# Kernel tuning notes

Hardware: AMD Instinct MI355X
Metric: run time of the kernel (lower is better)

Reference implementation:

```python
import math
import jax, jax.numpy as jnp
import numpy as np

B, S, HID = 2, 1024, 1024
NH, HD = 16, 64
WIN = 4096
CACHE = 3072
EPS = 1e-5


def _clinear(xr, xi, Wr, Wi, br, bi):
    # complex linear: (xr + i xi)(Wr + i Wi)^T + (br + i bi)
    yr = xr @ Wr.T - xi @ Wi.T + br
    yi = xr @ Wi.T + xi @ Wr.T + bi
    return yr, yi


def _forward(hidden_re, hidden_im, K_cache_re, K_cache_im, V_cache_re, V_cache_im,
             gamma, beta_re, beta_im,
             q_Wr, q_Wi, q_br, q_bi, k_Wr, k_Wi, k_br, k_bi,
             v_Wr, v_Wi, v_br, v_bi, o_Wr, o_Wi, o_br, o_bi):
    batch, seq, _ = hidden_re.shape
    # --- complex LayerNorm: center complex mean, normalize by sqrt(E|x-mu|^2) ---
    mur = hidden_re.mean(-1, keepdims=True)
    mui = hidden_im.mean(-1, keepdims=True)
    cr = hidden_re - mur
    ci = hidden_im - mui
    inv = jax.lax.rsqrt((cr * cr + ci * ci).mean(-1, keepdims=True) + EPS)
    nr = cr * inv * gamma + beta_re
    ni = ci * inv * gamma + beta_im
    # --- projections ---
    Qr, Qi = _clinear(nr, ni, q_Wr, q_Wi, q_br, q_bi)
    Kr, Ki = _clinear(nr, ni, k_Wr, k_Wi, k_br, k_bi)
    Vr, Vi = _clinear(nr, ni, v_Wr, v_Wi, v_br, v_bi)
    Qr = Qr.reshape(batch, seq, NH, HD)
    Qi = Qi.reshape(batch, seq, NH, HD)
    Kr = Kr.reshape(batch, seq, NH, HD)
    Ki = Ki.reshape(batch, seq, NH, HD)
    Vr = Vr.reshape(batch, seq, NH, HD)
    Vi = Vi.reshape(batch, seq, NH, HD)
    # --- KV cache concat + window eviction (static shapes) ---
    cache_len = K_cache_re.shape[1]
    Kr = jnp.concatenate([K_cache_re, Kr], axis=1)
    Ki = jnp.concatenate([K_cache_im, Ki], axis=1)
    Vr = jnp.concatenate([V_cache_re, Vr], axis=1)
    Vi = jnp.concatenate([V_cache_im, Vi], axis=1)
    total_kv = Kr.shape[1]
    if total_kv > WIN:
        drop = total_kv - WIN
        Kr, Ki, Vr, Vi = Kr[:, drop:], Ki[:, drop:], Vr[:, drop:], Vi[:, drop:]
        cache_len = max(0, cache_len - drop)
        total_kv = WIN
    # --- Hermitian scores: Re(Q K^H) = Qr.Kr + Qi.Ki ---
    scale = 1.0 / math.sqrt(HD)
    scores = (jnp.einsum('bshd,bthd->bhst', Qr, Kr)
              + jnp.einsum('bshd,bthd->bhst', Qi, Ki)) * scale
    rows = jnp.arange(seq)[:, None]
    cols = jnp.arange(total_kv)[None, :]
    allowed = cols <= rows + cache_len  # causal within current chunk, full cache visible
    scores = jnp.where(allowed, scores, jnp.float32(-1e30))
    weights = jax.nn.softmax(scores, axis=-1)  # [B,NH,S,T]
    outr = jnp.einsum('bhst,bthd->bshd', weights, Vr).reshape(batch, seq, NH * HD)
    outi = jnp.einsum('bhst,bthd->bshd', weights, Vi).reshape(batch, seq, NH * HD)
    dr, di = _clinear(outr, outi, o_Wr, o_Wi, o_br, o_bi)
    out_re = hidden_re + dr
    out_im = hidden_im + di
    new_K_re, new_K_im = Kr[:, -WIN:], Ki[:, -WIN:]
    new_V_re, new_V_im = Vr[:, -WIN:], Vi[:, -WIN:]
    return out_re, out_im, new_K_re, new_K_im, new_V_re, new_V_im


def setup_inputs() -> dict:
    key = jax.random.key(0)
    ks = jax.random.split(key, 16)
    w = 0.02
    d = {
        'hidden_re': jax.random.normal(ks[0], (B, S, HID), jnp.float32),
        'hidden_im': jax.random.normal(ks[1], (B, S, HID), jnp.float32),
        'K_cache_re': jax.random.normal(ks[2], (B, CACHE, NH, HD), jnp.float32),
        'K_cache_im': jax.random.normal(ks[3], (B, CACHE, NH, HD), jnp.float32),
        'V_cache_re': jax.random.normal(ks[4], (B, CACHE, NH, HD), jnp.float32),
        'V_cache_im': jax.random.normal(ks[5], (B, CACHE, NH, HD), jnp.float32),
        'gamma': jnp.ones((HID,), jnp.float32),
        'beta_re': jnp.zeros((HID,), jnp.float32),
        'beta_im': jnp.zeros((HID,), jnp.float32),
    }
    for i, p in enumerate(['q', 'k', 'v', 'o']):
        d[p + '_Wr'] = jax.random.normal(ks[6 + 2 * i], (HID, HID), jnp.float32) * w
        d[p + '_Wi'] = jax.random.normal(ks[7 + 2 * i], (HID, HID), jnp.float32) * w
        d[p + '_br'] = jnp.zeros((HID,), jnp.float32)
        d[p + '_bi'] = jnp.zeros((HID,), jnp.float32)
    return d


def reference(hidden_re, hidden_im, K_cache_re, K_cache_im, V_cache_re, V_cache_im,
              gamma, beta_re, beta_im,
              q_Wr, q_Wi, q_br, q_bi, k_Wr, k_Wi, k_br, k_bi,
              v_Wr, v_Wi, v_br, v_bi, o_Wr, o_Wi, o_br, o_bi):
    return _forward(hidden_re, hidden_im, K_cache_re, K_cache_im, V_cache_re, V_cache_im,
                    gamma, beta_re, beta_im,
                    q_Wr, q_Wi, q_br, q_bi, k_Wr, k_Wi, k_br, k_bi,
                    v_Wr, v_Wi, v_br, v_bi, o_Wr, o_Wi, o_br, o_bi)
```

## Files before the change

kernel.cpp:

```cpp
#include <hip/hip_runtime.h>
#include <hip/hip_bf16.h>
#include <cstdint>
#include <cstddef>

typedef __bf16 bf16x8 __attribute__((ext_vector_type(8)));
typedef float  f32x4  __attribute__((ext_vector_type(4)));

__device__ __forceinline__ unsigned short f2bf(float f) {
  union { float f; unsigned u; } v; v.f = f;
  unsigned u = v.u;
  u += 0x7FFFu + ((u >> 16) & 1u);
  return (unsigned short)(u >> 16);
}

struct alignas(16) US8 { unsigned short u[8]; };

__device__ __forceinline__ void g2lds16(const void* g, void* l) {
  __builtin_amdgcn_global_load_lds(
      (const __attribute__((address_space(1))) unsigned int*)g,
      (__attribute__((address_space(3))) unsigned int*)l, 16, 0, 0);
}

#define BB 2
#define SS 1024
#define HID 1024
#define NHH 16
#define HDD 64
#define TT 4096
#define CCH 3072

__global__ __launch_bounds__(256) void ln_kernel(
    const float* __restrict__ hre, const float* __restrict__ him,
    const float* __restrict__ gamma, const float* __restrict__ bre,
    const float* __restrict__ bim, unsigned short* __restrict__ Aln)
{
  int m = blockIdx.x;
  int tid = threadIdx.x;
  const float4 vr = ((const float4*)(hre + (size_t)m * HID))[tid];
  const float4 vi = ((const float4*)(him + (size_t)m * HID))[tid];
  float sr = vr.x + vr.y + vr.z + vr.w;
  float si = vi.x + vi.y + vi.z + vi.w;
  float sq = vr.x*vr.x + vr.y*vr.y + vr.z*vr.z + vr.w*vr.w
           + vi.x*vi.x + vi.y*vi.y + vi.z*vi.z + vi.w*vi.w;
  __shared__ float red[3][4];
  int lane = tid & 63, w = tid >> 6;
  for (int off = 32; off; off >>= 1) {
    sr += __shfl_down(sr, off, 64);
    si += __shfl_down(si, off, 64);
    sq += __shfl_down(sq, off, 64);
  }
  if (lane == 0) { red[0][w] = sr; red[1][w] = si; red[2][w] = sq; }
  __syncthreads();
  sr = red[0][0] + red[0][1] + red[0][2] + red[0][3];
  si = red[1][0] + red[1][1] + red[1][2] + red[1][3];
  sq = red[2][0] + red[2][1] + red[2][2] + red[2][3];
  float mur = sr * (1.f/1024.f), mui = si * (1.f/1024.f);
  float var = sq * (1.f/1024.f) - mur*mur - mui*mui;
  float inv = rsqrtf(var + 1e-5f);
  int k = tid * 4;
  float4 g  = ((const float4*)gamma)[tid];
  float4 br = ((const float4*)bre)[tid];
  float4 bi = ((const float4*)bim)[tid];
  ushort4 nr, ni;
  nr.x = f2bf((vr.x - mur) * inv * g.x + br.x);
  nr.y = f2bf((vr.y - mur) * inv * g.y + br.y);
  nr.z = f2bf((vr.z - mur) * inv * g.z + br.z);
  nr.w = f2bf((vr.w - mur) * inv * g.w + br.w);
  ni.x = f2bf((vi.x - mui) * inv * g.x + bi.x);
  ni.y = f2bf((vi.y - mui) * inv * g.y + bi.y);
  ni.z = f2bf((vi.z - mui) * inv * g.z + bi.z);
  ni.w = f2bf((vi.w - mui) * inv * g.w + bi.w);
  *(ushort4*)&Aln[(size_t)m * 2048 + k]        = nr;
  *(ushort4*)&Aln[(size_t)m * 2048 + 1024 + k] = ni;
}

__global__ __launch_bounds__(256) void wprep_kernel(
    const float* __restrict__ qWr, const float* __restrict__ qWi,
    const float* __restrict__ kWr, const float* __restrict__ kWi,
    const float* __restrict__ vWr, const float* __restrict__ vWi,
    const float* __restrict__ oWr, const float* __restrict__ oWi,
    unsigned short* __restrict__ Wc)
{
  int gid = blockIdx.x * 256 + threadIdx.x;
  int idx = gid * 8;
  int p   = idx >> 22;
  int rem = idx & 0x3FFFFF;
  int n   = rem >> 11;
  int k   = rem & 2047;
  const float* Wr; const float* Wi;
  switch (p) {
    case 0:  Wr = qWr; Wi = qWi; break;
    case 1:  Wr = kWr; Wi = kWi; break;
    case 2:  Wr = vWr; Wi = vWi; break;
    default: Wr = oWr; Wi = oWi; break;
  }
  const float* src; float sgn = 1.f;
  if (n < 1024) {
    if (k < 1024) src = Wr + (size_t)n * 1024 + k;
    else        { src = Wi + (size_t)n * 1024 + (k - 1024); sgn = -1.f; }
  } else {
    if (k < 1024) src = Wi + (size_t)(n - 1024) * 1024 + k;
    else          src = Wr + (size_t)(n - 1024) * 1024 + (k - 1024);
  }
  float4 a = ((const float4*)src)[0];
  float4 b = ((const float4*)src)[1];
  US8 o;
  o.u[0] = f2bf(a.x * sgn); o.u[1] = f2bf(a.y * sgn);
  o.u[2] = f2bf(a.z * sgn); o.u[3] = f2bf(a.w * sgn);
  o.u[4] = f2bf(b.x * sgn); o.u[5] = f2bf(b.y * sgn);
  o.u[6] = f2bf(b.z * sgn); o.u[7] = f2bf(b.w * sgn);
  *(US8*)&Wc[idx] = o;
}

__global__ __launch_bounds__(256) void bprep_kernel(
    const float* __restrict__ qbr, const float* __restrict__ qbi,
    const float* __restrict__ kbr, const float* __restrict__ kbi,
    const float* __restrict__ vbr, const float* __restrict__ vbi,
    const float* __restrict__ obr, const float* __restrict__ obi,
    float* __restrict__ bc)
{
  int idx = blockIdx.x * 256 + threadIdx.x;
  int p = idx >> 11, n = idx & 2047;
  const float* br; const float* bi;
  switch (p) {
    case 0:  br = qbr; bi = qbi; break;
    case 1:  br = kbr; bi = kbi; break;
    case 2:  br = vbr; bi = vbi; break;
    default: br = obr; bi = obi; break;
  }
  bc[idx] = (n < 1024) ? br[n] : bi[n - 1024];
}

__global__ __launch_bounds__(256) void gemm_bt_kernel(
    const unsigned short* __restrict__ A, const unsigned short* __restrict__ Bm,
    const float* __restrict__ bias, float* __restrict__ C, int Nstride, int K)
{
  __shared__ alignas(16) unsigned short As[128][32];
  __shared__ alignas(16) unsigned short Bs[128][32];
  int bm = blockIdx.y * 128;
  int bn = blockIdx.x * 128;
  int tid = threadIdx.x;
  int lane = tid & 63, w = tid >> 6;
  int wm = (w >> 1) * 64, wn = (w & 1) * 64;
  int l15 = lane & 15, q = lane >> 4;
  int lr = tid >> 2;
  int lc = (tid & 3) * 8;

  f32x4 acc[4][4] = {};

  for (int k0 = 0; k0 < K; k0 += 32) {
    *(float4*)&As[lr][lc]    = *(const float4*)&A [(size_t)(bm + lr)      * K + k0 + lc];
    *(float4*)&As[lr+64][lc] = *(const float4*)&A [(size_t)(bm + lr + 64) * K + k0 + lc];
    *(float4*)&Bs[lr][lc]    = *(const float4*)&Bm[(size_t)(bn + lr)      * K + k0 + lc];
    *(float4*)&Bs[lr+64][lc] = *(const float4*)&Bm[(size_t)(bn + lr + 64) * K + k0 + lc];
    __syncthreads();
    bf16x8 af[4], bfr[4];
#pragma unroll
    for (int i = 0; i < 4; i++) af[i]  = *(const bf16x8*)&As[wm + i*16 + l15][q*8];
#pragma unroll
    for (int i = 0; i < 4; i++) bfr[i] = *(const bf16x8*)&Bs[wn + i*16 + l15][q*8];
#pragma unroll
    for (int i = 0; i < 4; i++)
#pragma unroll
      for (int j = 0; j < 4; j++)
        acc[i][j] = __builtin_amdgcn_mfma_f32_16x16x32_bf16(af[i], bfr[j], acc[i][j], 0, 0, 0);
    __syncthreads();
  }

#pragma unroll
  for (int i = 0; i < 4; i++)
#pragma unroll
    for (int j = 0; j < 4; j++) {
      int n = bn + wn + j*16 + l15;
      float bv = bias[n];
#pragma unroll
      for (int r = 0; r < 4; r++) {
        int m = bm + wm + i*16 + q*4 + r;
        C[(size_t)m * Nstride + n] = acc[i][j][r] + bv;
      }
    }
}

__global__ __launch_bounds__(256) void gemm_oproj_kernel(
    const unsigned short* __restrict__ A, const unsigned short* __restrict__ Bm,
    const float* __restrict__ bias, const float* __restrict__ hre,
    const float* __restrict__ him, float* __restrict__ out)
{
  __shared__ alignas(16) unsigned short As[128][32];
  __shared__ alignas(16) unsigned short Bs[128][32];
  int bm = blockIdx.y * 128;
  int bn = blockIdx.x * 128;
  int tid = threadIdx.x;
  int lane = tid & 63, w = tid >> 6;
  int wm = (w >> 1) * 64, wn = (w & 1) * 64;
  int l15 = lane & 15, q = lane >> 4;
  int lr = tid >> 2;
  int lc = (tid & 3) * 8;
  const int K = 2048;

  f32x4 acc[4][4] = {};

  for (int k0 = 0; k0 < K; k0 += 32) {
    *(float4*)&As[lr][lc]    = *(const float4*)&A [(size_t)(bm + lr)      * K + k0 + lc];
    *(float4*)&As[lr+64][lc] = *(const float4*)&A [(size_t)(bm + lr + 64) * K + k0 + lc];
    *(float4*)&Bs[lr][lc]    = *(const float4*)&Bm[(size_t)(bn + lr)      * K + k0 + lc];
    *(float4*)&Bs[lr+64][lc] = *(const float4*)&Bm[(size_t)(bn + lr + 64) * K + k0 + lc];
    __syncthreads();
    bf16x8 af[4], bfr[4];
#pragma unroll
    for (int i = 0; i < 4; i++) af[i]  = *(const bf16x8*)&As[wm + i*16 + l15][q*8];
#pragma unroll
    for (int i = 0; i < 4; i++) bfr[i] = *(const bf16x8*)&Bs[wn + i*16 + l15][q*8];
#pragma unroll
    for (int i = 0; i < 4; i++)
#pragma unroll
      for (int j = 0; j < 4; j++)
        acc[i][j] = __builtin_amdgcn_mfma_f32_16x16x32_bf16(af[i], bfr[j], acc[i][j], 0, 0, 0);
    __syncthreads();
  }

#pragma unroll
  for (int i = 0; i < 4; i++)
#pragma unroll
    for (int j = 0; j < 4; j++) {
      int n = bn + wn + j*16 + l15;
      float bv = bias[n];
#pragma unroll
      for (int r = 0; r < 4; r++) {
        int m = bm + wm + i*16 + q*4 + r;
        float val = acc[i][j][r] + bv;
        if (n < 1024) out[(size_t)m * 1024 + n] = val + hre[(size_t)m * 1024 + n];
        else out[2097152 + (size_t)m * 1024 + (n - 1024)] = val + him[(size_t)m * 1024 + (n - 1024)];
      }
    }
}

__global__ __launch_bounds__(256) void pack_q_kernel(
    const float* __restrict__ Cqkv, unsigned short* __restrict__ Qp)
{
  int gid = blockIdx.x * 256 + threadIdx.x;
  int idx = gid * 4;
  int d2 = idx & 127;
  int s  = (idx >> 7) & 1023;
  int bh = idx >> 17;
  int b = bh >> 4, h = bh & 15;
  int d = d2 & 63;
  int col = (d2 < 64) ? (h*64 + d) : (1024 + h*64 + d);
  float4 v = *(const float4*)&Cqkv[((size_t)b * 1024 + s) * 6144 + col];
  ushort4 o;
  o.x = f2bf(v.x * 0.125f); o.y = f2bf(v.y * 0.125f);
  o.z = f2bf(v.z * 0.125f); o.w = f2bf(v.w * 0.125f);
  *(ushort4*)&Qp[idx] = o;
}

__global__ __launch_bounds__(256) void pack_kv_kernel(
    const float* __restrict__ c_re, const float* __restrict__ c_im,
    const float* __restrict__ Cqkv, int colbase,
    unsigned short* __restrict__ Kp,
    float* __restrict__ out_re, float* __restrict__ out_im)
{
  int gid = blockIdx.x * 256 + threadIdx.x;
  int idx = gid * 4;
  int d2 = idx & 127;
  int t  = (idx >> 7) & 4095;
  int bh = idx >> 19;
  int b = bh >> 4, h = bh & 15;
  int d = d2 & 63;
  bool im = d2 >= 64;
  float4 v;
  if (t < CCH) {
    const float* src = im ? c_im : c_re;
    v = *(const float4*)&src[(((size_t)b * CCH + t) * 16 + h) * 64 + d];
  } else {
    int col = colbase + (im ? (1024 + h*64 + d) : (h*64 + d));
    v = *(const float4*)&Cqkv[((size_t)b * 1024 + (t - CCH)) * 6144 + col];
  }
  if (Kp) {
    ushort4 o;
    o.x = f2bf(v.x); o.y = f2bf(v.y); o.z = f2bf(v.z); o.w = f2bf(v.w);
    *(ushort4*)&Kp[idx] = o;
  }
  float* dst = im ? out_im : out_re;
  *(float4*)&dst[(((size_t)b * 4096 + t) * 16 + h) * 64 + d] = v;
}

__global__ __launch_bounds__(256) void pack_vt_kernel(
    const float* __restrict__ Vc_re, const float* __restrict__ Vc_im,
    const float* __restrict__ Cqkv, unsigned short* __restrict__ Vt)
{
  __shared__ float Ts[64][136];
  const int ty = blockIdx.x & 63;
  const int bh = blockIdx.x >> 6;
  const int b = bh >> 4, h = bh & 15;
  const int t0 = ty * 64;
  const int tid = threadIdx.x;
#pragma unroll
  for (int rr = 0; rr < 8; rr++) {
    int j = rr * 256 + tid;
    int t_loc = j >> 5, c = j & 31;
    int d2 = c * 4;
    int t = t0 + t_loc;
    float4 v;
    if (t < CCH) {
      const float* src = (d2 < 64) ? Vc_re : Vc_im;
      int d = (d2 < 64) ? d2 : d2 - 64;
      v = *(const float4*)&src[(((size_t)b * CCH + t) * 16 + h) * 64 + d];
    } else {
      int col = 4096 + ((d2 < 64) ? (h*64 + d2) : (1024 + h*64 + d2 - 64));
      v = *(const float4*)&Cqkv[((size_t)b * 1024 + (t - CCH)) * 6144 + col];
    }
    *(float4*)&Ts[t_loc][d2] = v;
  }
  __syncthreads();
  const int d2 = tid >> 1, half = tid & 1;
  unsigned short tmp[32];
#pragma unroll
  for (int i = 0; i < 32; i++) tmp[i] = f2bf(Ts[half*32 + i][d2]);
  size_t dst = (size_t)bh * 128 * 4096 + (size_t)d2 * 4096 + t0 + half*32;
#pragma unroll
  for (int kq = 0; kq < 4; kq++)
    *(US8*)&Vt[dst + kq*8] = *(US8*)&tmp[kq*8];
}

__global__ __launch_bounds__(256) void attn_kernel(
    const unsigned short* __restrict__ Qp, const unsigned short* __restrict__ Kp,
    const unsigned short* __restrict__ Vt, float* __restrict__ Opart,
    float* __restrict__ Lpart)
{
  const int bh   = blockIdx.x;
  const int sblk = blockIdx.y;
  const int tpar = blockIdx.z;
  const int s0 = sblk * 128;
  const int tid = threadIdx.x;
  const int lane = tid & 63, w = tid >> 6;
  const int l15 = lane & 15, q = lane >> 4;

  __shared__ alignas(16) unsigned short Ks[2][64][128];
  __shared__ alignas(16) unsigned short Vs[2][128][64];
  __shared__ alignas(16) unsigned short Ps[4][32][64];

  bf16x8 qf[2][4];
#pragma unroll
  for (int mi = 0; mi < 2; mi++) {
    const size_t qb = ((size_t)bh * 1024 + s0 + w*32 + mi*16 + l15) * 128;
#pragma unroll
    for (int kc = 0; kc < 4; kc++)
      qf[mi][kc] = *(const bf16x8*)&Qp[qb + kc*32 + q*8];
  }

  f32x4 oacc[2][8] = {};
  float lsum[2][4] = {};

  const size_t kpb = (size_t)bh * 4096 * 128;
  const size_t vtb = (size_t)bh * 128 * 4096;
  const int n_tiles = 2*sblk + 50;
  const int n_safe  = n_tiles - 2;

  auto issue = [&](int buf, int t0) {
#pragma unroll
    for (int kk = 0; kk < 4; kk++) {
      int j = (w*4 + kk)*64 + lane;
      int r = j >> 4, p = j & 15, c = p ^ (r & 7);
      g2lds16(&Kp[kpb + (size_t)(t0 + r) * 128 + c*8],
              (unsigned short*)&Ks[buf][0][0] + (size_t)j * 8);
    }
#pragma unroll
    for (int kk = 0; kk < 4; kk++) {
      int j = (w*4 + kk)*64 + lane;
      int r = j >> 3, p = j & 7, c = p ^ (r & 7);
      g2lds16(&Vt[vtb + (size_t)r * 4096 + t0 + c*8],
              (unsigned short*)&Vs[buf][0][0] + (size_t)j * 8);
    }
  };

  int buf = 0;
  issue(0, tpar * 64);

  for (int it = tpar; it < n_tiles; it += 2) {
    __syncthreads();
    if (it + 2 < n_tiles) issue(buf ^ 1, (it + 2) * 64);

    f32x4 sacc[2][4] = {};
#pragma unroll
    for (int kc = 0; kc < 4; kc++) {
      bf16x8 kf[4];
#pragma unroll
      for (int nc = 0; nc < 4; nc++)
        kf[nc] = *(const bf16x8*)&Ks[buf][nc*16 + l15][((kc*4 + q) ^ (l15 & 7)) * 8];
#pragma unroll
      for (int mi = 0; mi < 2; mi++)
#pragma unroll
        for (int nc = 0; nc < 4; nc++)
          sacc[mi][nc] = __builtin_amdgcn_mfma_f32_16x16x32_bf16(qf[mi][kc], kf[nc], sacc[mi][nc], 0, 0, 0);
    }

    const bool safe = (it < n_safe);
    const int t0 = it << 6;
#pragma unroll
    for (int mi = 0; mi < 2; mi++)
#pragma unroll
      for (int r = 0; r < 4; r++) {
        const int rr = mi*16 + q*4 + r;
        const int rel = s0 + w*32 + rr + CCH - t0;
        float ls = 0.f;
#pragma unroll
        for (int nc = 0; nc < 4; nc++) {
          float p = __expf(sacc[mi][nc][r]);
          if (!safe && (nc*16 + l15 > rel)) p = 0.f;
          ls += p;
          int cch = ((nc*2 + (l15 >> 3)) ^ (rr & 7));
          Ps[w][rr][cch*8 + (l15 & 7)] = f2bf(p);
        }
        lsum[mi][r] += ls;
      }

#pragma unroll
    for (int kch = 0; kch < 2; kch++) {
      bf16x8 pf[2];
#pragma unroll
      for (int mi = 0; mi < 2; mi++) {
        int rr = mi*16 + l15;
        pf[mi] = *(const bf16x8*)&Ps[w][rr][((kch*4 + q) ^ (rr & 7)) * 8];
      }
#pragma unroll
      for (int dc = 0; dc < 8; dc++) {
        int d2 = dc*16 + l15;
        bf16x8 vfr = *(const bf16x8*)&Vs[buf][d2][((kch*4 + q) ^ (l15 & 7)) * 8];
#pragma unroll
        for (int mi = 0; mi < 2; mi++)
          oacc[mi][dc] = __builtin_amdgcn_mfma_f32_16x16x32_bf16(pf[mi], vfr, oacc[mi][dc], 0, 0, 0);
      }
    }
    buf ^= 1;
  }

  const size_t pb = ((size_t)tpar * 32 + bh) * 1024 + s0 + w*32;
#pragma unroll
  for (int mi = 0; mi < 2; mi++)
#pragma unroll
    for (int r = 0; r < 4; r++) {
      float l = lsum[mi][r];
      l += __shfl_xor(l, 1, 64);
      l += __shfl_xor(l, 2, 64);
      l += __shfl_xor(l, 4, 64);
      l += __shfl_xor(l, 8, 64);
      if (l15 == 0) Lpart[pb + mi*16 + q*4 + r] = l;
    }
#pragma unroll
  for (int mi = 0; mi < 2; mi++)
#pragma unroll
    for (int dc = 0; dc < 8; dc++)
#pragma unroll
      for (int r = 0; r < 4; r++)
        Opart[(pb + mi*16 + q*4 + r) * 128 + dc*16 + l15] = oacc[mi][dc][r];
}

__global__ __launch_bounds__(256) void attn_combine_kernel(
    const float* __restrict__ Opart, const float* __restrict__ Lpart,
    unsigned short* __restrict__ Ao)
{
  const size_t TS = 4194304ull;
  int gid = blockIdx.x * 256 + threadIdx.x;
  int idx = gid * 8;
  int m = idx >> 11, n0 = idx & 2047;
  int b = m >> 10, s = m & 1023;
  int h, d2_0;
  if (n0 < 1024) { h = n0 >> 6; d2_0 = n0 & 63; }
  else { h = (n0 - 1024) >> 6; d2_0 = 64 + ((n0 - 1024) & 63); }
  int bh = b*16 + h;
  size_t ob = ((size_t)bh * 1024 + s) * 128 + d2_0;
  float l0 = Lpart[(size_t)bh * 1024 + s];
  float l1 = Lpart[TS/128 + (size_t)bh * 1024 + s];
  float inv = 1.f / (l0 + l1);
  float4 x0 = *(const float4*)&Opart[ob];
  float4 x1 = *(const float4*)&Opart[ob + 4];
  float4 y0 = *(const float4*)&Opart[ob + TS];
  float4 y1 = *(const float4*)&Opart[ob + TS + 4];
  US8 o;
  o.u[0] = f2bf((x0.x + y0.x) * inv); o.u[1] = f2bf((x0.y + y0.y) * inv);
  o.u[2] = f2bf((x0.z + y0.z) * inv); o.u[3] = f2bf((x0.w + y0.w) * inv);
  o.u[4] = f2bf((x1.x + y1.x) * inv); o.u[5] = f2bf((x1.y + y1.y) * inv);
  o.u[6] = f2bf((x1.z + y1.z) * inv); o.u[7] = f2bf((x1.w + y1.w) * inv);
  *(US8*)&Ao[idx] = o;
}

extern "C" void kernel_launch(void* const* d_in, const int* in_sizes, int n_in,
                              void* d_out, int out_size, void* d_ws, size_t ws_size,
                              hipStream_t stream)
{
  (void)in_sizes; (void)n_in; (void)out_size; (void)ws_size;
  const float* hre = (const float*)d_in[0];
  const float* him = (const float*)d_in[1];
  const float* Kcr = (const float*)d_in[2];
  const float* Kci = (const float*)d_in[3];
  const float* Vcr = (const float*)d_in[4];
  const float* Vci = (const float*)d_in[5];
  const float* gamma = (const float*)d_in[6];
  const float* bre = (const float*)d_in[7];
  const float* bim = (const float*)d_in[8];
  const float* qWr = (const float*)d_in[9];
  const float* qWi = (const float*)d_in[10];
  const float* qbr = (const float*)d_in[11];
  const float* qbi = (const float*)d_in[12];
  const float* kWr = (const float*)d_in[13];
  const float* kWi = (const float*)d_in[14];
  const float* kbr = (const float*)d_in[15];
  const float* kbi = (const float*)d_in[16];
  const float* vWr = (const float*)d_in[17];
  const float* vWi = (const float*)d_in[18];
  const float* vbr = (const float*)d_in[19];
  const float* vbi = (const float*)d_in[20];
  const float* oWr = (const float*)d_in[21];
  const float* oWi = (const float*)d_in[22];
  const float* obr = (const float*)d_in[23];
  const float* obi = (const float*)d_in[24];
  float* out = (float*)d_out;

  char* ws = (char*)d_ws;
  size_t off = 0;
  auto carve = [&](size_t bytes) {
    char* p = ws + off;
    off += (bytes + 255) & ~(size_t)255;
    return p;
  };
  unsigned short* Aln = (unsigned short*)carve(2048ull * 2048 * 2);
  unsigned short* Wc  = (unsigned short*)carve(4ull * 2048 * 2048 * 2);
  float*          bc  = (float*)carve(4ull * 2048 * 4);
  float*          Cqkv= (float*)carve(2048ull * 6144 * 4);
  unsigned short* Qp  = (unsigned short*)carve(4194304ull * 2);
  unsigned short* Kp  = (unsigned short*)carve(16777216ull * 2);
  unsigned short* Vt  = (unsigned short*)carve(16777216ull * 2);
  unsigned short* Ao  = (unsigned short*)carve(2048ull * 2048 * 2);

  float* Opart = (float*)Cqkv;
  float* Lpart = (float*)Aln;

  float* out_Kre = out + 4194304;
  float* out_Kim = out + 4194304 + 8388608;
  float* out_Vre = out + 4194304 + 2 * 8388608;
  float* out_Vim = out + 4194304 + 3 * 8388608;

  hipLaunchKernelGGL(ln_kernel, dim3(2048), dim3(256), 0, stream,
                     hre, him, gamma, bre, bim, Aln);
  hipLaunchKernelGGL(wprep_kernel, dim3(8192), dim3(256), 0, stream,
                     qWr, qWi, kWr, kWi, vWr, vWi, oWr, oWi, Wc);
  hipLaunchKernelGGL(bprep_kernel, dim3(32), dim3(256), 0, stream,
                     qbr, qbi, kbr, kbi, vbr, vbi, obr, obi, bc);
  hipLaunchKernelGGL(gemm_bt_kernel, dim3(48, 16), dim3(256), 0, stream,
                     Aln, Wc, bc, Cqkv, 6144, 2048);
  hipLaunchKernelGGL(pack_q_kernel, dim3(4096), dim3(256), 0, stream, Cqkv, Qp);
  hipLaunchKernelGGL(pack_kv_kernel, dim3(16384), dim3(256), 0, stream,
                     Kcr, Kci, Cqkv, 2048, Kp, out_Kre, out_Kim);
  hipLaunchKernelGGL(pack_kv_kernel, dim3(16384), dim3(256), 0, stream,
                     Vcr, Vci, Cqkv, 4096, (unsigned short*)nullptr, out_Vre, out_Vim);
  hipLaunchKernelGGL(pack_vt_kernel, dim3(2048), dim3(256), 0, stream,
                     Vcr, Vci, Cqkv, Vt);
  hipLaunchKernelGGL(attn_kernel, dim3(32, 8, 2), dim3(256), 0, stream,
                     Qp, Kp, Vt, Opart, Lpart);
  hipLaunchKernelGGL(attn_combine_kernel, dim3(2048), dim3(256), 0, stream,
                     Opart, Lpart, Ao);
  hipLaunchKernelGGL(gemm_oproj_kernel, dim3(16, 16), dim3(256), 0, stream,
                     Ao, Wc + 3ull * 2048 * 2048, bc + 3 * 2048, hre, him, out);
}
```

Measured before the change: 610.8 us.

## Use direct global-to-LDS loads in GEMMs, fuse V packing, split attention three ways

The projection GEMMs now load tiles with global_load_lds instead of staging through registers. The separate V cache-copy kernel is folded into the V transpose kernel, so V is read once. Attention splits KV into three partitions instead of two and drops LDS double-buffering in favour of single-buffered tiles with an extra barrier. Partial outputs are stored as bf16 and P is truncated rather than rounded. This cuts launches and traffic and raises parallelism, but loses load/compute overlap in attention and adds rounding error in the partial sums.

```diff
diff --git a/kernel.cpp b/kernel.cpp
--- a/kernel.cpp
+++ b/kernel.cpp
@@ -11,6 +11,9 @@
   unsigned u = v.u;
   u += 0x7FFFu + ((u >> 16) & 1u);
   return (unsigned short)(u >> 16);
+}
+__device__ __forceinline__ float bf2f(unsigned short u) {
+  union { unsigned u; float f; } v; v.u = ((unsigned)u) << 16; return v.f;
 }
 
 struct alignas(16) US8 { unsigned short u[8]; };
@@ -28,6 +31,7 @@
 #define HDD 64
 #define TT 4096
 #define CCH 3072
+#define TPAR 3
 
 __global__ __launch_bounds__(256) void ln_kernel(
     const float* __restrict__ hre, const float* __restrict__ him,
@@ -143,16 +147,20 @@
   int lane = tid & 63, w = tid >> 6;
   int wm = (w >> 1) * 64, wn = (w & 1) * 64;
   int l15 = lane & 15, q = lane >> 4;
-  int lr = tid >> 2;
-  int lc = (tid & 3) * 8;
+  int sr = tid >> 2;
+  int sc = (tid & 3) * 8;
+  char* ldsA  = (char*)As + (size_t)w * 1024;
+  char* ldsA2 = ldsA + 4096;
+  char* ldsB  = (char*)Bs + (size_t)w * 1024;
+  char* ldsB2 = ldsB + 4096;
 
   f32x4 acc[4][4] = {};
 
   for (int k0 = 0; k0 < K; k0 += 32) {
-    *(float4*)&As[lr][lc]    = *(const float4*)&A [(size_t)(bm + lr)      * K + k0 + lc];
-    *(float4*)&As[lr+64][lc] = *(const float4*)&A [(size_t)(bm + lr + 64) * K + k0 + lc];
-    *(float4*)&Bs[lr][lc]    = *(const float4*)&Bm[(size_t)(bn + lr)      * K + k0 + lc];
-    *(float4*)&Bs[lr+64][lc] = *(const float4*)&Bm[(size_t)(bn + lr + 64) * K + k0 + lc];
+    g2lds16(&A [(size_t)(bm + sr)      * K + k0 + sc], ldsA);
+    g2lds16(&A [(size_t)(bm + 64 + sr) * K + k0 + sc], ldsA2);
+    g2lds16(&Bm[(size_t)(bn + sr)      * K + k0 + sc], ldsB);
+    g2lds16(&Bm[(size_t)(bn + 64 + sr) * K + k0 + sc], ldsB2);
     __syncthreads();
     bf16x8 af[4], bfr[4];
 #pragma unroll
@@ -194,17 +202,21 @@
   int lane = tid & 63, w = tid >> 6;
   int wm = (w >> 1) * 64, wn = (w & 1) * 64;
   int l15 = lane & 15, q = lane >> 4;
-  int lr = tid >> 2;
-  int lc = (tid & 3) * 8;
+  int sr = tid >> 2;
+  int sc = (tid & 3) * 8;
   const int K = 2048;
+  char* ldsA  = (char*)As + (size_t)w * 1024;
+  char* ldsA2 = ldsA + 4096;
+  char* ldsB  = (char*)Bs + (size_t)w * 1024;
+  char* ldsB2 = ldsB + 4096;
 
   f32x4 acc[4][4] = {};
 
   for (int k0 = 0; k0 < K; k0 += 32) {
-    *(float4*)&As[lr][lc]    = *(const float4*)&A [(size_t)(bm + lr)      * K + k0 + lc];
-    *(float4*)&As[lr+64][lc] = *(const float4*)&A [(size_t)(bm + lr + 64) * K + k0 + lc];
-    *(float4*)&Bs[lr][lc]    = *(const float4*)&Bm[(size_t)(bn + lr)      * K + k0 + lc];
-    *(float4*)&Bs[lr+64][lc] = *(const float4*)&Bm[(size_t)(bn + lr + 64) * K + k0 + lc];
+    g2lds16(&A [(size_t)(bm + sr)      * K + k0 + sc], ldsA);
+    g2lds16(&A [(size_t)(bm + 64 + sr) * K + k0 + sc], ldsA2);
+    g2lds16(&Bm[(size_t)(bn + sr)      * K + k0 + sc], ldsB);
+    g2lds16(&Bm[(size_t)(bn + 64 + sr) * K + k0 + sc], ldsB2);
     __syncthreads();
     bf16x8 af[4], bfr[4];
 #pragma unroll
@@ -253,9 +265,9 @@
   *(ushort4*)&Qp[idx] = o;
 }
 
-__global__ __launch_bounds__(256) void pack_kv_kernel(
+__global__ __launch_bounds__(256) void pack_k_kernel(
     const float* __restrict__ c_re, const float* __restrict__ c_im,
-    const float* __restrict__ Cqkv, int colbase,
+    const float* __restrict__ Cqkv,
     unsigned short* __restrict__ Kp,
     float* __restrict__ out_re, float* __restrict__ out_im)
 {
@@ -272,21 +284,20 @@
     const float* src = im ? c_im : c_re;
     v = *(const float4*)&src[(((size_t)b * CCH + t) * 16 + h) * 64 + d];
   } else {
-    int col = colbase + (im ? (1024 + h*64 + d) : (h*64 + d));
+    int col = 2048 + (im ? (1024 + h*64 + d) : (h*64 + d));
     v = *(const float4*)&Cqkv[((size_t)b * 1024 + (t - CCH)) * 6144 + col];
   }
-  if (Kp) {
-    ushort4 o;
-    o.x = f2bf(v.x); o.y = f2bf(v.y); o.z = f2bf(v.z); o.w = f2bf(v.w);
-    *(ushort4*)&Kp[idx] = o;
-  }
+  ushort4 o;
+  o.x = f2bf(v.x); o.y = f2bf(v.y); o.z = f2bf(v.z); o.w = f2bf(v.w);
+  *(ushort4*)&Kp[idx] = o;
   float* dst = im ? out_im : out_re;
   *(float4*)&dst[(((size_t)b * 4096 + t) * 16 + h) * 64 + d] = v;
 }
 
-__global__ __launch_bounds__(256) void pack_vt_kernel(
+__global__ __launch_bounds__(256) void pack_v_kernel(
     const float* __restrict__ Vc_re, const float* __restrict__ Vc_im,
-    const float* __restrict__ Cqkv, unsigned short* __restrict__ Vt)
+    const float* __restrict__ Cqkv, unsigned short* __restrict__ Vt,
+    float* __restrict__ out_re, float* __restrict__ out_im)
 {
   __shared__ float Ts[64][136];
   const int ty = blockIdx.x & 63;
@@ -310,6 +321,9 @@
       v = *(const float4*)&Cqkv[((size_t)b * 1024 + (t - CCH)) * 6144 + col];
     }
     *(float4*)&Ts[t_loc][d2] = v;
+    float* dst = (d2 < 64) ? out_re : out_im;
+    int d = (d2 < 64) ? d2 : d2 - 64;
+    *(float4*)&dst[(((size_t)b * 4096 + t) * 16 + h) * 64 + d] = v;
   }
   __syncthreads();
   const int d2 = tid >> 1, half = tid & 1;
@@ -324,7 +338,7 @@
 
 __global__ __launch_bounds__(256) void attn_kernel(
     const unsigned short* __restrict__ Qp, const unsigned short* __restrict__ Kp,
-    const unsigned short* __restrict__ Vt, float* __restrict__ Opart,
+    const unsigned short* __restrict__ Vt, unsigned short* __restrict__ Opart,
     float* __restrict__ Lpart)
 {
   const int bh   = blockIdx.x;
@@ -335,8 +349,8 @@
   const int lane = tid & 63, w = tid >> 6;
   const int l15 = lane & 15, q = lane >> 4;
 
-  __shared__ alignas(16) unsigned short Ks[2][64][128];
-  __shared__ alignas(16) unsigned short Vs[2][128][64];
+  __shared__ alignas(16) unsigned short Ks[64][128];
+  __shared__ alignas(16) unsigned short Vs[128][64];
   __shared__ alignas(16) unsigned short Ps[4][32][64];
 
   bf16x8 qf[2][4];
@@ -356,29 +370,26 @@
   const int n_tiles = 2*sblk + 50;
   const int n_safe  = n_tiles - 2;
 
-  auto issue = [&](int buf, int t0) {
+  auto issue = [&](int t0) {
 #pragma unroll
     for (int kk = 0; kk < 4; kk++) {
       int j = (w*4 + kk)*64 + lane;
       int r = j >> 4, p = j & 15, c = p ^ (r & 7);
       g2lds16(&Kp[kpb + (size_t)(t0 + r) * 128 + c*8],
-              (unsigned short*)&Ks[buf][0][0] + (size_t)j * 8);
+              (unsigned short*)&Ks[0][0] + (size_t)j * 8);
     }
 #pragma unroll
     for (int kk = 0; kk < 4; kk++) {
       int j = (w*4 + kk)*64 + lane;
       int r = j >> 3, p = j & 7, c = p ^ (r & 7);
       g2lds16(&Vt[vtb + (size_t)r * 4096 + t0 + c*8],
-              (unsigned short*)&Vs[buf][0][0] + (size_t)j * 8);
+              (unsigned short*)&Vs[0][0] + (size_t)j * 8);
     }
   };
 
-  int buf = 0;
-  issue(0, tpar * 64);
-
-  for (int it = tpar; it < n_tiles; it += 2) {
+  for (int it = tpar; it < n_tiles; it += TPAR) {
+    issue(it << 6);
     __syncthreads();
-    if (it + 2 < n_tiles) issue(buf ^ 1, (it + 2) * 64);
 
     f32x4 sacc[2][4] = {};
 #pragma unroll
@@ -386,7 +397,7 @@
       bf16x8 kf[4];
 #pragma unroll
       for (int nc = 0; nc < 4; nc++)
-        kf[nc] = *(const bf16x8*)&Ks[buf][nc*16 + l15][((kc*4 + q) ^ (l15 & 7)) * 8];
+        kf[nc] = *(const bf16x8*)&Ks[nc*16 + l15][((kc*4 + q) ^ (l15 & 7)) * 8];
 #pragma unroll
       for (int mi = 0; mi < 2; mi++)
 #pragma unroll
@@ -409,7 +420,7 @@
           if (!safe && (nc*16 + l15 > rel)) p = 0.f;
           ls += p;
           int cch = ((nc*2 + (l15 >> 3)) ^ (rr & 7));
-          Ps[w][rr][cch*8 + (l15 & 7)] = f2bf(p);
+          Ps[w][rr][cch*8 + (l15 & 7)] = (unsigned short)(__float_as_uint(p) >> 16);
         }
         lsum[mi][r] += ls;
       }
@@ -425,13 +436,13 @@
 #pragma unroll
       for (int dc = 0; dc < 8; dc++) {
         int d2 = dc*16 + l15;
-        bf16x8 vfr = *(const bf16x8*)&Vs[buf][d2][((kch*4 + q) ^ (l15 & 7)) * 8];
+        bf16x8 vfr = *(const bf16x8*)&Vs[d2][((kch*4 + q) ^ (l15 & 7)) * 8];
 #pragma unroll
         for (int mi = 0; mi < 2; mi++)
           oacc[mi][dc] = __builtin_amdgcn_mfma_f32_16x16x32_bf16(pf[mi], vfr, oacc[mi][dc], 0, 0, 0);
       }
     }
-    buf ^= 1;
+    __syncthreads();
   }
 
   const size_t pb = ((size_t)tpar * 32 + bh) * 1024 + s0 + w*32;
@@ -452,11 +463,11 @@
     for (int dc = 0; dc < 8; dc++)
 #pragma unroll
       for (int r = 0; r < 4; r++)
-        Opart[(pb + mi*16 + q*4 + r) * 128 + dc*16 + l15] = oacc[mi][dc][r];
+        Opart[(pb + mi*16 + q*4 + r) * 128 + dc*16 + l15] = f2bf(oacc[mi][dc][r]);
 }
 
 __global__ __launch_bounds__(256) void attn_combine_kernel(
-    const float* __restrict__ Opart, const float* __restrict__ Lpart,
+    const unsigned short* __restrict__ Opart, const float* __restrict__ Lpart,
     unsigned short* __restrict__ Ao)
 {
   const size_t TS = 4194304ull;
@@ -469,18 +480,19 @@
   else { h = (n0 - 1024) >> 6; d2_0 = 64 + ((n0 - 1024) & 63); }
   int bh = b*16 + h;
   size_t ob = ((size_t)bh * 1024 + s) * 128 + d2_0;
-  float l0 = Lpart[(size_t)bh * 1024 + s];
-  float l1 = Lpart[TS/128 + (size_t)bh * 1024 + s];
-  float inv = 1.f / (l0 + l1);
-  float4 x0 = *(const float4*)&Opart[ob];
-  float4 x1 = *(const float4*)&Opart[ob + 4];
-  float4 y0 = *(const float4*)&Opart[ob + TS];
-  float4 y1 = *(const float4*)&Opart[ob + TS + 4];
+  size_t lb = (size_t)bh * 1024 + s;
+  float l = Lpart[lb] + Lpart[32768 + lb] + Lpart[65536 + lb];
+  float inv = 1.f / l;
+  float acc[8] = {};
+#pragma unroll
+  for (int tp = 0; tp < TPAR; tp++) {
+    US8 x = *(const US8*)&Opart[ob + (size_t)tp * TS];
+#pragma unroll
+    for (int i = 0; i < 8; i++) acc[i] += bf2f(x.u[i]);
+  }
   US8 o;
-  o.u[0] = f2bf((x0.x + y0.x) * inv); o.u[1] = f2bf((x0.y + y0.y) * inv);
-  o.u[2] = f2bf((x0.z + y0.z) * inv); o.u[3] = f2bf((x0.w + y0.w) * inv);
-  o.u[4] = f2bf((x1.x + y1.x) * inv); o.u[5] = f2bf((x1.y + y1.y) * inv);
-  o.u[6] = f2bf((x1.z + y1.z) * inv); o.u[7] = f2bf((x1.w + y1.w) * inv);
+#pragma unroll
+  for (int i = 0; i < 8; i++) o.u[i] = f2bf(acc[i] * inv);
   *(US8*)&Ao[idx] = o;
 }
 
@@ -532,8 +544,8 @@
   unsigned short* Vt  = (unsigned short*)carve(16777216ull * 2);
   unsigned short* Ao  = (unsigned short*)carve(2048ull * 2048 * 2);
 
-  float* Opart = (float*)Cqkv;
-  float* Lpart = (float*)Aln;
+  unsigned short* Opart = (unsigned short*)Cqkv;
+  float*          Lpart = (float*)Aln;
 
   float* out_Kre = out + 4194304;
   float* out_Kim = out + 4194304 + 8388608;
@@ -549,13 +561,11 @@
   hipLaunchKernelGGL(gemm_bt_kernel, dim3(48, 16), dim3(256), 0, stream,
                      Aln, Wc, bc, Cqkv, 6144, 2048);
   hipLaunchKernelGGL(pack_q_kernel, dim3(4096), dim3(256), 0, stream, Cqkv, Qp);
-  hipLaunchKernelGGL(pack_kv_kernel, dim3(16384), dim3(256), 0, stream,
-                     Kcr, Kci, Cqkv, 2048, Kp, out_Kre, out_Kim);
-  hipLaunchKernelGGL(pack_kv_kernel, dim3(16384), dim3(256), 0, stream,
-                     Vcr, Vci, Cqkv, 4096, (unsigned short*)nullptr, out_Vre, out_Vim);
-  hipLaunchKernelGGL(pack_vt_kernel, dim3(2048), dim3(256), 0, stream,
-                     Vcr, Vci, Cqkv, Vt);
-  hipLaunchKernelGGL(attn_kernel, dim3(32, 8, 2), dim3(256), 0, stream,
+  hipLaunchKernelGGL(pack_k_kernel, dim3(16384), dim3(256), 0, stream,
+                     Kcr, Kci, Cqkv, Kp, out_Kre, out_Kim);
+  hipLaunchKernelGGL(pack_v_kernel, dim3(2048), dim3(256), 0, stream,
+                     Vcr, Vci, Cqkv, Vt, out_Vre, out_Vim);
+  hipLaunchKernelGGL(attn_kernel, dim3(32, 8, TPAR), dim3(256), 0, stream,
                      Qp, Kp, Vt, Opart, Lpart);
   hipLaunchKernelGGL(attn_combine_kernel, dim3(2048), dim3(256), 0, stream,
                      Opart, Lpart, Ao);
```

New measurement: 631.5 us. 3.4% more time.
